# Optimization experiments

Hardware: AMD Instinct MI355X
Metric: run time of the kernel (lower is better)

## Reference

```python
import jax, jax.numpy as jnp
import numpy as np

N = 50000      # nodes
E = 800000     # edges (before self-loops)
IN_F = 128     # in_feature
HID = 64       # hidden_feature (out_channels per head)
HEADS = 3
NEG_SLOPE = 0.2  # PyG GATConv default negative_slope


def setup_inputs() -> dict:
    key = jax.random.key(0)
    ks = jax.random.split(key, 12)
    x = jax.random.normal(ks[0], (N, IN_F), dtype=jnp.float32)
    src = jax.random.randint(ks[1], (E,), 0, N, dtype=jnp.int32)
    off = jax.random.randint(ks[2], (E,), 1, N, dtype=jnp.int32)
    dst = (src + off) % N  # guarantees no pre-existing self-loops
    edge_index = jnp.stack([src, dst]).astype(jnp.int32)

    def glorot(k, shape, fan_in):
        return (jax.random.normal(k, shape, dtype=jnp.float32)
                / np.float32(np.sqrt(fan_in)))

    W1 = glorot(ks[3], (IN_F, HEADS * HID), IN_F)
    att_src1 = glorot(ks[4], (HEADS, HID), HID)
    att_dst1 = glorot(ks[5], (HEADS, HID), HID)
    bias1 = jnp.zeros((HID,), jnp.float32)
    W2 = glorot(ks[6], (HID, HEADS * HID), HID)
    att_src2 = glorot(ks[7], (HEADS, HID), HID)
    att_dst2 = glorot(ks[8], (HEADS, HID), HID)
    bias2 = jnp.zeros((HID,), jnp.float32)
    return dict(x=x, edge_index=edge_index,
                W1=W1, att_src1=att_src1, att_dst1=att_dst1, bias1=bias1,
                W2=W2, att_src2=att_src2, att_dst2=att_dst2, bias2=bias2)


def gat_layer(x, W, a_src, a_dst, bias, src, dst):
    """PyG GATConv: heads=HEADS, concat=False (mean over heads), self-loops added."""
    h = (x @ W).reshape(-1, HEADS, HID)              # [N, H, C]
    alpha_src = jnp.einsum('nhc,hc->nh', h, a_src)   # [N, H]
    alpha_dst = jnp.einsum('nhc,hc->nh', h, a_dst)   # [N, H]
    loop = jnp.arange(N, dtype=src.dtype)
    s = jnp.concatenate([src, loop])                 # add self-loops
    d = jnp.concatenate([dst, loop])
    e = jax.nn.leaky_relu(alpha_src[s] + alpha_dst[d], NEG_SLOPE)  # [E+N, H]
    # segment softmax over edges grouped by destination node
    m = jax.ops.segment_max(e, d, num_segments=N)    # [N, H]; every node has a self-loop
    p = jnp.exp(e - m[d])
    denom = jax.ops.segment_sum(p, d, num_segments=N)
    alpha = p / (denom[d] + 1e-16)                   # [E+N, H]
    out = jax.ops.segment_sum(alpha[:, :, None] * h[s], d, num_segments=N)  # [N, H, C]
    return out.mean(axis=1) + bias                   # concat=False -> head mean


def reference(x, edge_index, W1, att_src1, att_dst1, bias1,
              W2, att_src2, att_dst2, bias2):
    src, dst = edge_index[0], edge_index[1]
    h1 = gat_layer(x, W1, att_src1, att_dst1, bias1, src, dst)
    h1 = jax.nn.relu(h1)  # dropout(p=0.2) is identity in eval mode
    return gat_layer(h1, W2, att_src2, att_dst2, bias2, src, dst)
```

## Files before the change

kernel.cpp:

```cpp
#include <hip/hip_runtime.h>
#include <hip/hip_fp16.h>
#include <math.h>

#define N_NODES 50000
#define N_EDGES 800000
#define NEG 0.2f


__global__ void zero_kernel(int* a, int n) {
    int i = blockIdx.x * blockDim.x + threadIdx.x;
    if (i < n) a[i] = 0;
}

__global__ void count_kernel(const int* __restrict__ dst, int* cnt, int E) {
    int i = blockIdx.x * blockDim.x + threadIdx.x;
    if (i < E) atomicAdd(&cnt[dst[i]], 1);
}

__global__ void scan1_kernel(const int* __restrict__ cnt, int* rowptr, int* partials, int n) {
    __shared__ int sh[256];
    int tid = threadIdx.x;
    int i = blockIdx.x * 256 + tid;
    int v = (i < n) ? cnt[i] : 0;
    sh[tid] = v;
    __syncthreads();
    for (int off = 1; off < 256; off <<= 1) {
        int t = (tid >= off) ? sh[tid - off] : 0;
        __syncthreads();
        sh[tid] += t;
        __syncthreads();
    }
    if (i < n) rowptr[i] = sh[tid] - v;
    if (tid == 255) partials[blockIdx.x] = sh[255];
}

__global__ void scan2_kernel(int* partials, int nb) {
    __shared__ int sh[256];
    int tid = threadIdx.x;
    int v = (tid < nb) ? partials[tid] : 0;
    sh[tid] = v;
    __syncthreads();
    for (int off = 1; off < 256; off <<= 1) {
        int t = (tid >= off) ? sh[tid - off] : 0;
        __syncthreads();
        sh[tid] += t;
        __syncthreads();
    }
    if (tid < nb) partials[tid] = sh[tid] - v;
}

__global__ void scan3_kernel(int* rowptr, const int* __restrict__ partials, int n) {
    int i = blockIdx.x * blockDim.x + threadIdx.x;
    if (i < n) rowptr[i] += partials[i >> 8];
    if (i == 0) rowptr[n] = N_EDGES;
}

__global__ void fill_kernel(const int* __restrict__ src, const int* __restrict__ dst,
                            const int* __restrict__ rowptr, int* cnt, int* col, int E) {
    int i = blockIdx.x * blockDim.x + threadIdx.x;
    if (i < E) {
        int d = dst[i];
        int pos = rowptr[d] + atomicSub(&cnt[d], 1) - 1;
        col[pos] = src[i];
    }
}

template <int K>
__global__ __launch_bounds__(256) void gemm_kernel(const float* __restrict__ A,
                                                   const float* __restrict__ W,
                                                   __half* __restrict__ out,
                                                   const float* __restrict__ att_src,
                                                   const float* __restrict__ att_dst,
                                                   float* __restrict__ as4,
                                                   float* __restrict__ ad4,
                                                   float* __restrict__ wself4, int rows) {
    constexpr int KT = 32;
    __shared__ float xs[KT][68];
    __shared__ float ws[KT][192];
    int tid = threadIdx.x;
    int tx = tid & 15;
    int ty = tid >> 4;
    int row0 = blockIdx.x * 64;

    float acc[4][12];
#pragma unroll
    for (int r = 0; r < 4; ++r)
#pragma unroll
        for (int c = 0; c < 12; ++c) acc[r][c] = 0.f;

    for (int kt = 0; kt < K; kt += KT) {
#pragma unroll
        for (int idx = tid; idx < 64 * KT; idx += 256) {
            int r = idx >> 5, kk = idx & 31;
            int rr = row0 + r;
            xs[kk][r] = (rr < rows) ? A[rr * K + kt + kk] : 0.f;
        }
#pragma unroll
        for (int idx = tid; idx < KT * 192; idx += 256) {
            int kk = idx / 192, c = idx - kk * 192;
            ws[kk][c] = W[(kt + kk) * 192 + c];
        }
        __syncthreads();
#pragma unroll 2
        for (int k = 0; k < KT; ++k) {
            float4 a4 = *(const float4*)&xs[k][ty * 4];
            float4 w0 = *(const float4*)&ws[k][tx * 12];
            float4 w1 = *(const float4*)&ws[k][tx * 12 + 4];
            float4 w2 = *(const float4*)&ws[k][tx * 12 + 8];
            float av[4] = {a4.x, a4.y, a4.z, a4.w};
            float wv[12] = {w0.x, w0.y, w0.z, w0.w, w1.x, w1.y, w1.z, w1.w,
                            w2.x, w2.y, w2.z, w2.w};
#pragma unroll
            for (int r = 0; r < 4; ++r)
#pragma unroll
                for (int c = 0; c < 12; ++c) acc[r][c] += av[r] * wv[c];
        }
        __syncthreads();
    }

    float asr[12], adr[12];
#pragma unroll
    for (int c = 0; c < 12; ++c) {
        asr[c] = att_src[tx * 12 + c];
        adr[c] = att_dst[tx * 12 + c];
    }
#pragma unroll
    for (int r = 0; r < 4; ++r) {
        int rr = row0 + ty * 4 + r;
        bool ok = rr < rows;
        if (ok) {
            __half2* o = (__half2*)(out + (size_t)rr * 192 + tx * 12);
#pragma unroll
            for (int c = 0; c < 6; ++c)
                o[c] = __floats2half2_rn(acc[r][2 * c], acc[r][2 * c + 1]);
        }
        float s0 = 0, s1 = 0, s2 = 0, d0 = 0, d1 = 0, d2 = 0;
#pragma unroll
        for (int c = 0; c < 12; ++c) {
            int cc = tx * 12 + c;
            float p = acc[r][c] * asr[c];
            float q = acc[r][c] * adr[c];
            if (cc < 64)       { s0 += p; d0 += q; }
            else if (cc < 128) { s1 += p; d1 += q; }
            else               { s2 += p; d2 += q; }
        }
        for (int off = 1; off < 16; off <<= 1) {
            s0 += __shfl_xor(s0, off); s1 += __shfl_xor(s1, off); s2 += __shfl_xor(s2, off);
            d0 += __shfl_xor(d0, off); d1 += __shfl_xor(d1, off); d2 += __shfl_xor(d2, off);
        }
        if (tx == 0 && ok) {
            as4[rr * 4 + 0] = s0; as4[rr * 4 + 1] = s1; as4[rr * 4 + 2] = s2;
            ad4[rr * 4 + 0] = d0; ad4[rr * 4 + 1] = d1; ad4[rr * 4 + 2] = d2;
            float v0 = s0 + d0; v0 = v0 > 0.f ? v0 : NEG * v0;
            float v1 = s1 + d1; v1 = v1 > 0.f ? v1 : NEG * v1;
            float v2 = s2 + d2; v2 = v2 > 0.f ? v2 : NEG * v2;
            wself4[rr * 4 + 0] = __expf(v0);
            wself4[rr * 4 + 1] = __expf(v1);
            wself4[rr * 4 + 2] = __expf(v2);
        }
    }
}

template <bool RELU>
__global__ __launch_bounds__(256) void aggregate_kernel(const __half* __restrict__ h,
                                                        const float* __restrict__ as_,
                                                        const float* __restrict__ ad4,
                                                        const float* __restrict__ wself4,
                                                        const float* __restrict__ bias,
                                                        const int* __restrict__ rowptr,
                                                        const int* __restrict__ col,
                                                        float* __restrict__ out, int n) {
    constexpr int U = 8;
    __shared__ float sh[4][192];
    int wid = (int)((blockIdx.x * blockDim.x + threadIdx.x) >> 6);
    int l = threadIdx.x & 63;
    int wv = threadIdx.x >> 6;
    bool valid = wid < n;
    int d = valid ? wid : 0;
    if (valid && l < 48) {
        int hl = l >> 4;
        int r0 = rowptr[d], r1 = rowptr[d + 1];
        float adh = ad4[d * 4 + hl];
        float w = wself4[d * 4 + hl];
        float2 sraw = *(const float2*)(h + (size_t)d * 192 + l * 4);
        float2 s01 = __half22float2(*(__half2*)&sraw.x);
        float2 s23 = __half22float2(*(__half2*)&sraw.y);
        float ax = w * s01.x, ay = w * s01.y, az = w * s23.x, aw = w * s23.y;
        float den = w;

        for (int j = r0; j < r1; j += U) {
            int s[U];
            bool act[U];
            float av[U];
            float2 g[U];
#pragma unroll
            for (int u = 0; u < U; ++u) {
                int jj = j + u;
                act[u] = jj < r1;
                s[u] = act[u] ? col[jj] : 0;
            }
#pragma unroll
            for (int u = 0; u < U; ++u) {
                float t = as_[s[u] * 4 + hl];
                av[u] = act[u] ? t : -1e30f;
            }
#pragma unroll
            for (int u = 0; u < U; ++u)
                g[u] = *(const float2*)(h + (size_t)s[u] * 192 + l * 4);
#pragma unroll
            for (int u = 0; u < U; ++u) {
                float v = av[u] + adh;
                v = v > 0.f ? v : NEG * v;
                float we = __expf(v);
                float2 g01 = __half22float2(*(__half2*)&g[u].x);
                float2 g23 = __half22float2(*(__half2*)&g[u].y);
                den += we;
                ax += we * g01.x;
                ay += we * g01.y;
                az += we * g23.x;
                aw += we * g23.y;
            }
        }
        float r = 1.f / den;
        float4 o = {ax * r, ay * r, az * r, aw * r};
        *(float4*)&sh[wv][l * 4] = o;
    }
    __syncthreads();
    if (valid) {
        float o = (sh[wv][l] + sh[wv][64 + l] + sh[wv][128 + l]) * (1.f / 3.f) + bias[l];
        if (RELU) o = fmaxf(o, 0.f);
        out[(size_t)d * 64 + l] = o;
    }
}

extern "C" void kernel_launch(void* const* d_in, const int* in_sizes, int n_in,
                              void* d_out, int out_size, void* d_ws, size_t ws_size,
                              hipStream_t stream) {
    const float* x = (const float*)d_in[0];
    const int* ei = (const int*)d_in[1];
    const float* W1 = (const float*)d_in[2];
    const float* att_s1 = (const float*)d_in[3];
    const float* att_d1 = (const float*)d_in[4];
    const float* b1 = (const float*)d_in[5];
    const float* W2 = (const float*)d_in[6];
    const float* att_s2 = (const float*)d_in[7];
    const float* att_d2 = (const float*)d_in[8];
    const float* b2 = (const float*)d_in[9];
    const int* src = ei;
    const int* dst = ei + N_EDGES;

    __half* h16 = (__half*)d_ws;
    float* as4 = (float*)(h16 + (size_t)N_NODES * 192);
    float* ad4 = as4 + N_NODES * 4;
    float* wself4 = ad4 + N_NODES * 4;
    int* cnt = (int*)(wself4 + N_NODES * 4);
    int* rowptr = cnt + N_NODES;
    int* col = rowptr + N_NODES + 1;
    int* partials = col + N_EDGES;

    float* outf = (float*)d_out;
    const int NB = (N_NODES + 255) / 256;

    zero_kernel<<<(N_NODES + 255) / 256, 256, 0, stream>>>(cnt, N_NODES);
    count_kernel<<<(N_EDGES + 255) / 256, 256, 0, stream>>>(dst, cnt, N_EDGES);
    scan1_kernel<<<NB, 256, 0, stream>>>(cnt, rowptr, partials, N_NODES);
    scan2_kernel<<<1, 256, 0, stream>>>(partials, NB);
    scan3_kernel<<<NB, 256, 0, stream>>>(rowptr, partials, N_NODES);
    fill_kernel<<<(N_EDGES + 255) / 256, 256, 0, stream>>>(src, dst, rowptr, cnt, col, N_EDGES);

    gemm_kernel<128><<<(N_NODES + 63) / 64, 256, 0, stream>>>(x, W1, h16, att_s1, att_d1,
                                                              as4, ad4, wself4, N_NODES);
    aggregate_kernel<true><<<(N_NODES + 3) / 4, 256, 0, stream>>>(h16, as4, ad4, wself4, b1,
                                                                  rowptr, col, outf, N_NODES);

    gemm_kernel<64><<<(N_NODES + 63) / 64, 256, 0, stream>>>(outf, W2, h16, att_s2, att_d2,
                                                             as4, ad4, wself4, N_NODES);
    aggregate_kernel<false><<<(N_NODES + 3) / 4, 256, 0, stream>>>(h16, as4, ad4, wself4, b2,
                                                                   rowptr, col, outf, N_NODES);
}
```

Baseline: 364.2 us.

## Use MFMA fp16 GEMM and sort CSR rows by edge id

Replaces the scalar fp32 tiled GEMM with an MFMA 16x16x32 fp16 kernel, which uses a pre-transposed fp16 weight copy held in LDS and stages output through LDS for coalesced stores. It also records original edge ids during CSR fill and adds a per-row sort kernel that makes neighbor order deterministic. The sort is extra work, mainly for determinism or accuracy rather than speed. It adds two small transpose kernels and casts activations to fp16 before the matmul, which lowers precision.

```diff
diff --git a/kernel.cpp b/kernel.cpp
--- a/kernel.cpp
+++ b/kernel.cpp
@@ -1,10 +1,14 @@
 #include <hip/hip_runtime.h>
 #include <hip/hip_fp16.h>
 #include <math.h>
+#include <limits.h>
 
 #define N_NODES 50000
 #define N_EDGES 800000
 #define NEG 0.2f
+
+typedef _Float16 half8 __attribute__((ext_vector_type(8)));
+typedef float floatx4 __attribute__((ext_vector_type(4)));
 
 
 __global__ void zero_kernel(int* a, int n) {
@@ -56,108 +60,158 @@
 }
 
 __global__ void fill_kernel(const int* __restrict__ src, const int* __restrict__ dst,
-                            const int* __restrict__ rowptr, int* cnt, int* col, int E) {
+                            const int* __restrict__ rowptr, int* cnt, int* col, int* eidp, int E) {
     int i = blockIdx.x * blockDim.x + threadIdx.x;
     if (i < E) {
         int d = dst[i];
         int pos = rowptr[d] + atomicSub(&cnt[d], 1) - 1;
         col[pos] = src[i];
+        eidp[pos] = i;
+    }
+}
+
+__global__ void sortrow_kernel(const int* __restrict__ rowptr, int* col, int* eidp, int n) {
+    int wid = (int)((blockIdx.x * blockDim.x + threadIdx.x) >> 6);
+    int lane = threadIdx.x & 63;
+    if (wid >= n) return;
+    int r0 = rowptr[wid], r1 = rowptr[wid + 1];
+    int deg = r1 - r0;
+    if (deg <= 1) return;
+    if (deg <= 64) {
+        int key = (lane < deg) ? eidp[r0 + lane] : INT_MAX;
+        int val = (lane < deg) ? col[r0 + lane] : 0;
+#pragma unroll
+        for (int k = 2; k <= 64; k <<= 1) {
+#pragma unroll
+            for (int j = k >> 1; j > 0; j >>= 1) {
+                int pk = __shfl_xor(key, j);
+                int pv = __shfl_xor(val, j);
+                bool up = ((lane & k) == 0);
+                bool lower = ((lane & j) == 0);
+                bool take = lower ? ((pk < key) == up) : ((pk > key) == up);
+                if (take) { key = pk; val = pv; }
+            }
+        }
+        if (lane < deg) col[r0 + lane] = val;
+    } else if (lane == 0) {
+        for (int i = r0 + 1; i < r1; ++i) {
+            int ke = eidp[i], kv = col[i];
+            int j = i - 1;
+            while (j >= r0 && eidp[j] > ke) {
+                eidp[j + 1] = eidp[j];
+                col[j + 1] = col[j];
+                --j;
+            }
+            eidp[j + 1] = ke;
+            col[j + 1] = kv;
+        }
     }
 }
 
 template <int K>
-__global__ __launch_bounds__(256) void gemm_kernel(const float* __restrict__ A,
-                                                   const float* __restrict__ W,
-                                                   __half* __restrict__ out,
-                                                   const float* __restrict__ att_src,
-                                                   const float* __restrict__ att_dst,
-                                                   float* __restrict__ as4,
-                                                   float* __restrict__ ad4,
-                                                   float* __restrict__ wself4, int rows) {
-    constexpr int KT = 32;
-    __shared__ float xs[KT][68];
-    __shared__ float ws[KT][192];
+__global__ void wtrans_kernel(const float* __restrict__ W, __half* __restrict__ wt) {
+    int idx = blockIdx.x * blockDim.x + threadIdx.x;
+    if (idx < 192 * K) {
+        int n = idx / K, k = idx - n * K;
+        wt[idx] = __float2half(W[k * 192 + n]);
+    }
+}
+
+template <int K>
+__global__ __launch_bounds__(256) void mfma_gemm_kernel(const float* __restrict__ A,
+                                                        const __half* __restrict__ wt,
+                                                        __half* __restrict__ out,
+                                                        const float* __restrict__ att_src,
+                                                        const float* __restrict__ att_dst,
+                                                        float* __restrict__ as4,
+                                                        float* __restrict__ ad4,
+                                                        float* __restrict__ wself4, int rows) {
+    constexpr int KP = K + 8;
+    __shared__ __align__(16) __half lds[192 * KP];
     int tid = threadIdx.x;
-    int tx = tid & 15;
-    int ty = tid >> 4;
-    int row0 = blockIdx.x * 64;
-
-    float acc[4][12];
-#pragma unroll
-    for (int r = 0; r < 4; ++r)
-#pragma unroll
-        for (int c = 0; c < 12; ++c) acc[r][c] = 0.f;
-
-    for (int kt = 0; kt < K; kt += KT) {
-#pragma unroll
-        for (int idx = tid; idx < 64 * KT; idx += 256) {
-            int r = idx >> 5, kk = idx & 31;
-            int rr = row0 + r;
-            xs[kk][r] = (rr < rows) ? A[rr * K + kt + kk] : 0.f;
-        }
-#pragma unroll
-        for (int idx = tid; idx < KT * 192; idx += 256) {
-            int kk = idx / 192, c = idx - kk * 192;
-            ws[kk][c] = W[(kt + kk) * 192 + c];
-        }
-        __syncthreads();
-#pragma unroll 2
-        for (int k = 0; k < KT; ++k) {
-            float4 a4 = *(const float4*)&xs[k][ty * 4];
-            float4 w0 = *(const float4*)&ws[k][tx * 12];
-            float4 w1 = *(const float4*)&ws[k][tx * 12 + 4];
-            float4 w2 = *(const float4*)&ws[k][tx * 12 + 8];
-            float av[4] = {a4.x, a4.y, a4.z, a4.w};
-            float wv[12] = {w0.x, w0.y, w0.z, w0.w, w1.x, w1.y, w1.z, w1.w,
-                            w2.x, w2.y, w2.z, w2.w};
-#pragma unroll
-            for (int r = 0; r < 4; ++r)
-#pragma unroll
-                for (int c = 0; c < 12; ++c) acc[r][c] += av[r] * wv[c];
-        }
-        __syncthreads();
-    }
-
-    float asr[12], adr[12];
+    int lane = tid & 63;
+    int wv = tid >> 6;
+    int ln = lane & 15;
+    int q = lane >> 4;
+
+    for (int idx = tid; idx < 192 * (K / 8); idx += 256) {
+        int n = idx / (K / 8), kk = (idx % (K / 8)) * 8;
+        *(float4*)(lds + n * KP + kk) = *(const float4*)(wt + n * K + kk);
+    }
+
+    int m0 = blockIdx.x * 64 + wv * 16;
+    int m = m0 + ln;
+    int mc = m < rows ? m : 0;
+    half8 afr[K / 32];
+#pragma unroll
+    for (int kt = 0; kt < K / 32; ++kt) {
+        float4 a0 = *(const float4*)(A + (size_t)mc * K + kt * 32 + q * 8);
+        float4 a1 = *(const float4*)(A + (size_t)mc * K + kt * 32 + q * 8 + 4);
+        half8 f;
+        f[0] = (_Float16)a0.x; f[1] = (_Float16)a0.y; f[2] = (_Float16)a0.z; f[3] = (_Float16)a0.w;
+        f[4] = (_Float16)a1.x; f[5] = (_Float16)a1.y; f[6] = (_Float16)a1.z; f[7] = (_Float16)a1.w;
+        afr[kt] = f;
+    }
+
+    __syncthreads();
+
+    floatx4 acc[12];
+#pragma unroll
+    for (int c = 0; c < 12; ++c) acc[c] = (floatx4){0.f, 0.f, 0.f, 0.f};
+
+#pragma unroll
+    for (int kt = 0; kt < K / 32; ++kt) {
+#pragma unroll
+        for (int c = 0; c < 12; ++c) {
+            half8 b = *(const half8*)(lds + (c * 16 + ln) * KP + kt * 32 + q * 8);
+            acc[c] = __builtin_amdgcn_mfma_f32_16x16x32_f16(afr[kt], b, acc[c], 0, 0, 0);
+        }
+    }
+
+    float asv[12], adv[12];
 #pragma unroll
     for (int c = 0; c < 12; ++c) {
-        asr[c] = att_src[tx * 12 + c];
-        adr[c] = att_dst[tx * 12 + c];
+        asv[c] = att_src[c * 16 + ln];
+        adv[c] = att_dst[c * 16 + ln];
     }
 #pragma unroll
     for (int r = 0; r < 4; ++r) {
-        int rr = row0 + ty * 4 + r;
-        bool ok = rr < rows;
-        if (ok) {
-            __half2* o = (__half2*)(out + (size_t)rr * 192 + tx * 12);
-#pragma unroll
-            for (int c = 0; c < 6; ++c)
-                o[c] = __floats2half2_rn(acc[r][2 * c], acc[r][2 * c + 1]);
-        }
         float s0 = 0, s1 = 0, s2 = 0, d0 = 0, d1 = 0, d2 = 0;
 #pragma unroll
-        for (int c = 0; c < 12; ++c) {
-            int cc = tx * 12 + c;
-            float p = acc[r][c] * asr[c];
-            float q = acc[r][c] * adr[c];
-            if (cc < 64)       { s0 += p; d0 += q; }
-            else if (cc < 128) { s1 += p; d1 += q; }
-            else               { s2 += p; d2 += q; }
-        }
+        for (int c = 0; c < 4; ++c) { s0 += acc[c][r] * asv[c]; d0 += acc[c][r] * adv[c]; }
+#pragma unroll
+        for (int c = 4; c < 8; ++c) { s1 += acc[c][r] * asv[c]; d1 += acc[c][r] * adv[c]; }
+#pragma unroll
+        for (int c = 8; c < 12; ++c) { s2 += acc[c][r] * asv[c]; d2 += acc[c][r] * adv[c]; }
         for (int off = 1; off < 16; off <<= 1) {
             s0 += __shfl_xor(s0, off); s1 += __shfl_xor(s1, off); s2 += __shfl_xor(s2, off);
             d0 += __shfl_xor(d0, off); d1 += __shfl_xor(d1, off); d2 += __shfl_xor(d2, off);
         }
-        if (tx == 0 && ok) {
-            as4[rr * 4 + 0] = s0; as4[rr * 4 + 1] = s1; as4[rr * 4 + 2] = s2;
-            ad4[rr * 4 + 0] = d0; ad4[rr * 4 + 1] = d1; ad4[rr * 4 + 2] = d2;
+        int row = m0 + q * 4 + r;
+        if (ln == 0 && row < rows) {
+            as4[row * 4 + 0] = s0; as4[row * 4 + 1] = s1; as4[row * 4 + 2] = s2;
+            ad4[row * 4 + 0] = d0; ad4[row * 4 + 1] = d1; ad4[row * 4 + 2] = d2;
             float v0 = s0 + d0; v0 = v0 > 0.f ? v0 : NEG * v0;
             float v1 = s1 + d1; v1 = v1 > 0.f ? v1 : NEG * v1;
             float v2 = s2 + d2; v2 = v2 > 0.f ? v2 : NEG * v2;
-            wself4[rr * 4 + 0] = __expf(v0);
-            wself4[rr * 4 + 1] = __expf(v1);
-            wself4[rr * 4 + 2] = __expf(v2);
-        }
+            wself4[row * 4 + 0] = __expf(v0);
+            wself4[row * 4 + 1] = __expf(v1);
+            wself4[row * 4 + 2] = __expf(v2);
+        }
+    }
+
+    __syncthreads();
+#pragma unroll
+    for (int c = 0; c < 12; ++c)
+#pragma unroll
+        for (int r = 0; r < 4; ++r)
+            lds[(wv * 16 + q * 4 + r) * 192 + c * 16 + ln] = __float2half(acc[c][r]);
+    __syncthreads();
+    int row0 = blockIdx.x * 64;
+    for (int idx = tid; idx < 1536; idx += 256) {
+        int row = (idx * 8) / 192, off = (idx * 8) % 192;
+        if (row0 + row < rows)
+            *(float4*)(out + (size_t)(row0 + row) * 192 + off) = *(float4*)(lds + row * 192 + off);
     }
 }
 
@@ -250,31 +304,38 @@
     const int* dst = ei + N_EDGES;
 
     __half* h16 = (__half*)d_ws;
-    float* as4 = (float*)(h16 + (size_t)N_NODES * 192);
+    __half* wt1 = h16 + (size_t)N_NODES * 192;
+    __half* wt2 = wt1 + 192 * 128;
+    float* as4 = (float*)(wt2 + 192 * 64);
     float* ad4 = as4 + N_NODES * 4;
     float* wself4 = ad4 + N_NODES * 4;
     int* cnt = (int*)(wself4 + N_NODES * 4);
     int* rowptr = cnt + N_NODES;
     int* col = rowptr + N_NODES + 1;
-    int* partials = col + N_EDGES;
+    int* eidp = col + N_EDGES;
+    int* partials = eidp + N_EDGES;
 
     float* outf = (float*)d_out;
     const int NB = (N_NODES + 255) / 256;
+
+    wtrans_kernel<128><<<(192 * 128 + 255) / 256, 256, 0, stream>>>(W1, wt1);
+    wtrans_kernel<64><<<(192 * 64 + 255) / 256, 256, 0, stream>>>(W2, wt2);
 
     zero_kernel<<<(N_NODES + 255) / 256, 256, 0, stream>>>(cnt, N_NODES);
     count_kernel<<<(N_EDGES + 255) / 256, 256, 0, stream>>>(dst, cnt, N_EDGES);
     scan1_kernel<<<NB, 256, 0, stream>>>(cnt, rowptr, partials, N_NODES);
     scan2_kernel<<<1, 256, 0, stream>>>(partials, NB);
     scan3_kernel<<<NB, 256, 0, stream>>>(rowptr, partials, N_NODES);
-    fill_kernel<<<(N_EDGES + 255) / 256, 256, 0, stream>>>(src, dst, rowptr, cnt, col, N_EDGES);
-
-    gemm_kernel<128><<<(N_NODES + 63) / 64, 256, 0, stream>>>(x, W1, h16, att_s1, att_d1,
-                                                              as4, ad4, wself4, N_NODES);
+    fill_kernel<<<(N_EDGES + 255) / 256, 256, 0, stream>>>(src, dst, rowptr, cnt, col, eidp, N_EDGES);
+    sortrow_kernel<<<(N_NODES + 3) / 4, 256, 0, stream>>>(rowptr, col, eidp, N_NODES);
+
+    mfma_gemm_kernel<128><<<(N_NODES + 63) / 64, 256, 0, stream>>>(x, wt1, h16, att_s1, att_d1,
+                                                                   as4, ad4, wself4, N_NODES);
     aggregate_kernel<true><<<(N_NODES + 3) / 4, 256, 0, stream>>>(h16, as4, ad4, wself4, b1,
                                                                   rowptr, col, outf, N_NODES);
 
-    gemm_kernel<64><<<(N_NODES + 63) / 64, 256, 0, stream>>>(outf, W2, h16, att_s2, att_d2,
-                                                             as4, ad4, wself4, N_NODES);
+    mfma_gemm_kernel<64><<<(N_NODES + 63) / 64, 256, 0, stream>>>(outf, wt2, h16, att_s2, att_d2,
+                                                                  as4, ad4, wself4, N_NODES);
     aggregate_kernel<false><<<(N_NODES + 3) / 4, 256, 0, stream>>>(h16, as4, ad4, wself4, b2,
                                                                    rowptr, col, outf, N_NODES);
 }
```

New measurement: 363.8 us. Within noise of the previous version (-0.1%).
